# Optimization experiments

Measured on AMD Instinct MI355X. Metric: run time of the kernel, lower is better.

The kernel has to match this reference:

```python
import jax, jax.numpy as jnp
import numpy as np

N = 10000       # nodes
E = 160000      # edges
D_IN = 256      # in_channels (node feature dim)
H1, C = 8, 32   # conv1: 8 heads x 32 -> 256; conv2: 1 head x 32
MSG = 128       # msg_dim
TD = 128        # time encoder out_channels
ED = MSG + TD   # edge_dim = 256
HC1 = H1 * C    # 256


def _lin(key, shape, scale=0.05):
    return jax.random.normal(key, shape, dtype=jnp.float32) * scale


def setup_inputs() -> dict:
    key = jax.random.key(0)
    ks = jax.random.split(key, 32)
    inp = {}
    inp["x"] = jax.random.normal(ks[0], (N, D_IN), dtype=jnp.float32)
    inp["last_update"] = jax.random.uniform(ks[1], (N,), jnp.float32, 0.0, 1000.0)
    inp["edge_index"] = jax.random.randint(ks[2], (2, E), 0, N)
    inp["t"] = jax.random.uniform(ks[3], (E,), jnp.float32, 0.0, 1000.0)
    inp["msg"] = jax.random.normal(ks[4], (E, MSG), dtype=jnp.float32)
    # TimeEncoder: Linear(1, TD) then cos
    inp["time_w"] = _lin(ks[5], (TD, 1), 0.1)
    inp["time_b"] = jnp.zeros((TD,), jnp.float32)
    # conv1 (TransformerConv in=256, heads=8, per-head 32, edge_dim=256, concat=True)
    inp["Wq1"] = _lin(ks[6], (D_IN, HC1)); inp["bq1"] = jnp.zeros((HC1,), jnp.float32)
    inp["Wk1"] = _lin(ks[7], (D_IN, HC1)); inp["bk1"] = jnp.zeros((HC1,), jnp.float32)
    inp["Wv1"] = _lin(ks[8], (D_IN, HC1)); inp["bv1"] = jnp.zeros((HC1,), jnp.float32)
    inp["We1"] = _lin(ks[9], (ED, HC1))   # lin_edge has no bias in PyG
    inp["Ws1"] = _lin(ks[10], (D_IN, HC1)); inp["bs1"] = jnp.zeros((HC1,), jnp.float32)
    # conv2 (in=256, heads=1, per-head 32, concat=False)
    inp["Wq2"] = _lin(ks[11], (HC1, C)); inp["bq2"] = jnp.zeros((C,), jnp.float32)
    inp["Wk2"] = _lin(ks[12], (HC1, C)); inp["bk2"] = jnp.zeros((C,), jnp.float32)
    inp["Wv2"] = _lin(ks[13], (HC1, C)); inp["bv2"] = jnp.zeros((C,), jnp.float32)
    inp["We2"] = _lin(ks[14], (ED, C))
    inp["Ws2"] = _lin(ks[15], (HC1, C)); inp["bs2"] = jnp.zeros((C,), jnp.float32)
    return inp


def transformer_conv(x, src, dst, edge_attr, Wq, bq, Wk, bk, Wv, bv, We, Ws, bs, heads, ch, concat):
    n = x.shape[0]
    q = (x @ Wq + bq).reshape(n, heads, ch)
    k = (x @ Wk + bk).reshape(n, heads, ch)
    v = (x @ Wv + bv).reshape(n, heads, ch)
    e = (edge_attr @ We).reshape(-1, heads, ch)       # [E,H,C]
    ke = k[src] + e                                    # key_j + edge
    ve = v[src] + e                                    # value_j + edge
    alpha = jnp.einsum('ehc,ehc->eh', q[dst], ke) / jnp.sqrt(jnp.float32(ch))
    # segment softmax over incoming edges of each destination node
    amax = jax.ops.segment_max(alpha, dst, num_segments=n)   # -inf for empty segs
    ex = jnp.exp(alpha - amax[dst])
    den = jax.ops.segment_sum(ex, dst, num_segments=n)
    attn = ex / (den[dst] + 1e-16)                     # [E,H]
    out = jax.ops.segment_sum(attn[:, :, None] * ve, dst, num_segments=n)  # [N,H,C]
    out = out.reshape(n, heads * ch) if concat else out.mean(axis=1)
    return out + (x @ Ws + bs)                         # root skip connection


def reference(x, last_update, edge_index, t, msg, time_w, time_b,
              Wq1, bq1, Wk1, bk1, Wv1, bv1, We1, Ws1, bs1,
              Wq2, bq2, Wk2, bk2, Wv2, bv2, We2, Ws2, bs2):
    src, dst = edge_index[0], edge_index[1]
    rel_t = last_update[src] - t                       # [E]
    rel_t_enc = jnp.cos(rel_t[:, None] * time_w[:, 0][None, :] + time_b)  # [E,TD]
    edge_attr = jnp.concatenate([rel_t_enc, msg], axis=-1)                # [E,ED]
    h = jax.nn.relu(transformer_conv(x, src, dst, edge_attr,
                                     Wq1, bq1, Wk1, bk1, Wv1, bv1, We1, Ws1, bs1,
                                     H1, C, True))
    out = jax.nn.relu(transformer_conv(h, src, dst, edge_attr,
                                       Wq2, bq2, Wk2, bk2, Wv2, bv2, We2, Ws2, bs2,
                                       1, C, False))
    return out
```

## Files before the change

### kernel.cpp

```cpp
#include <hip/hip_runtime.h>
#include <math.h>

#define N_NODES 10000
#define N_EDGES 160000
#define RT1 157
#define RTE 2500
#define CONVX_T (RT1 * 64 * 32)
#define MAXSEG 16
#define SEGSTRIDE 576

static inline int ceildiv(int a, int b) { return (a + b - 1) / b; }

typedef float f32x4 __attribute__((ext_vector_type(4)));
typedef short bf16x8 __attribute__((ext_vector_type(8)));

__device__ __forceinline__ unsigned short f2bf(float f) {
  unsigned int u = __builtin_bit_cast(unsigned int, f);
  u += 0x7FFFu + ((u >> 16) & 1u);
  return (unsigned short)(u >> 16);
}
__device__ __forceinline__ float bf2f(unsigned short h) {
  unsigned int u = ((unsigned int)h) << 16;
  return __builtin_bit_cast(float, u);
}

__global__ void count_kernel(const int* __restrict__ dstp, int* __restrict__ deg, int E) {
  for (int i = blockIdx.x * blockDim.x + threadIdx.x; i < E; i += gridDim.x * blockDim.x)
    atomicAdd(&deg[dstp[i]], 1);
}

__global__ void scan_kernel(const int* __restrict__ deg, int* __restrict__ rowptr, int n) {
  __shared__ int part[1024];
  const int tid = threadIdx.x;
  const int CHK = 10;
  int base = tid * CHK;
  int loc[CHK];
  int s = 0;
#pragma unroll
  for (int j = 0; j < CHK; ++j) {
    int idx = base + j;
    int v = (idx < n) ? deg[idx] : 0;
    loc[j] = s; s += v;
  }
  part[tid] = s;
  __syncthreads();
  for (int off = 1; off < 1024; off <<= 1) {
    int y = (tid >= off) ? part[tid - off] : 0;
    __syncthreads();
    part[tid] += y;
    __syncthreads();
  }
  int pre = tid ? part[tid - 1] : 0;
#pragma unroll
  for (int j = 0; j < CHK; ++j) {
    int idx = base + j;
    if (idx < n) rowptr[idx] = pre + loc[j];
  }
  if (tid == 1023) rowptr[n] = part[1023];
}

__global__ void scatter_kernel(const float* __restrict__ lu, const float* __restrict__ tt,
                               const int* __restrict__ srcp, const int* __restrict__ dstp,
                               const int* __restrict__ rowptr, int* __restrict__ fill,
                               int* __restrict__ srcs, int* __restrict__ dsts,
                               int* __restrict__ eidA, float* __restrict__ rel_s, int E) {
  for (int e = blockIdx.x * blockDim.x + threadIdx.x; e < E; e += gridDim.x * blockDim.x) {
    int d = dstp[e], s = srcp[e];
    int pos = atomicAdd(&fill[d], 1);
    int slot = rowptr[d] + pos;
    srcs[slot] = s;
    dsts[slot] = d;
    eidA[slot] = e;
    rel_s[slot] = lu[s] - tt[e];
  }
}

__device__ __forceinline__ void wstore(const float* __restrict__ W, unsigned short* __restrict__ out,
                                       int Nin, int n_off, int NFtot, int k, int c) {
  int gc = n_off + c;
  int ks=k>>5, kg=(k>>3)&3, j=k&7, nf=gc>>4, ic=gc&15;
  out[(size_t)(ks*NFtot+nf)*512 + (ic+16*kg)*8 + j] = f2bf(W[(size_t)k*Nin + c]);
}

__global__ void conv_all_kernel(const float* __restrict__ x, unsigned short* __restrict__ xa,
                                const float* Wq1, const float* Wk1, const float* Wv1, const float* Ws1,
                                const float* We1, const float* Wq2, const float* Wk2, const float* Wv2,
                                const float* Ws2, const float* We2,
                                const float* bq1, const float* bk1, const float* bv1, const float* bs1,
                                const float* bq2, const float* bk2, const float* bv2, const float* bs2,
                                unsigned short* W1f, unsigned short* We1f, unsigned short* W2f,
                                unsigned short* We2f, float* bcat1, float* bcat2) {
  int t0 = blockIdx.x * blockDim.x + threadIdx.x;
  if (t0 < CONVX_T) {
    int i = t0 >> 5, k8 = t0 & 31;
    union { uint4 q; unsigned short s[8]; } u;
    if (i < N_NODES) {
      const float4* px = (const float4*)(x + (size_t)i * 256 + k8 * 8);
      float4 f0 = px[0], f1 = px[1];
      u.s[0]=f2bf(f0.x); u.s[1]=f2bf(f0.y); u.s[2]=f2bf(f0.z); u.s[3]=f2bf(f0.w);
      u.s[4]=f2bf(f1.x); u.s[5]=f2bf(f1.y); u.s[6]=f2bf(f1.z); u.s[7]=f2bf(f1.w);
    } else {
      u.q = make_uint4(0,0,0,0);
    }
    int rt=i>>6, rf=(i>>4)&3, ir=i&15, ks=k8>>2, kg=k8&3;
    *(uint4*)&xa[(size_t)rt*16384 + ks*2048 + rf*512 + (ir+16*kg)*8] = u.q;
    return;
  }
  int t = t0 - CONVX_T;
  if (t < 262144) {
    int w = t >> 16, r = t & 65535, k = r >> 8, c = r & 255;
    const float* W = (w == 0) ? Wq1 : (w == 1) ? Wk1 : (w == 2) ? Wv1 : Ws1;
    wstore(W, W1f, 256, w * 256, 64, k, c);
  } else if (t < 327680) {
    int r = t - 262144, k = r >> 8, c = r & 255;
    wstore(We1, We1f, 256, 0, 16, k, c);
  } else if (t < 360448) {
    int r = t - 327680, w = r >> 13, r2 = r & 8191, k = r2 >> 5, c = r2 & 31;
    const float* W = (w == 0) ? Wq2 : (w == 1) ? Wk2 : (w == 2) ? Wv2 : Ws2;
    wstore(W, W2f, 32, w * 32, 8, k, c);
  } else if (t < 368640) {
    int r = t - 360448, k = r >> 5, c = r & 31;
    wstore(We2, We2f, 32, 0, 4, k, c);
  } else if (t < 369792) {
    int r = t - 368640;
    if (r < 1024) {
      const float* b = (r < 256) ? bq1 : (r < 512) ? bk1 : (r < 768) ? bv1 : bs1;
      bcat1[r] = b[r & 255];
    } else {
      int r2 = r - 1024;
      const float* b = (r2 < 32) ? bq2 : (r2 < 64) ? bk2 : (r2 < 96) ? bv2 : bs2;
      bcat2[r2] = b[r2 & 31];
    }
  }
}

__global__ __launch_bounds__(512, 4)
void node1_gemm(const unsigned short* __restrict__ xa, const unsigned short* __restrict__ W1f,
                const float* __restrict__ bcat1, float* __restrict__ qf,
                unsigned short* __restrict__ kvb, float* __restrict__ sf) {
  __shared__ char ldsraw[32768];
  uint4* lds4 = (uint4*)ldsraw;
  const int tid = threadIdx.x;
  const int wid = tid >> 6, lane = tid & 63;
  const int fr0 = (lane >> 4) * 4;
  const int fc0 = lane & 15;
  const int rt0 = blockIdx.x % RT1;
  const int y = blockIdx.x / RT1;
  const int phase = rt0 & 7;

#pragma unroll
  for (int s = 0; s < 4; ++s)
    lds4[tid + s * 512] = *(const uint4*)(xa + (size_t)rt0 * 16384 + (size_t)(tid + s * 512) * 8);
  __syncthreads();

  f32x4 acc[4][2];
#pragma unroll
  for (int i = 0; i < 4; ++i)
#pragma unroll
    for (int j = 0; j < 2; ++j) acc[i][j] = (f32x4){0.f, 0.f, 0.f, 0.f};

  bf16x8 aN0, aN1, aN2, aN3, bN0, bN1;
  {
    const int ks = phase;
    aN0 = *(const bf16x8*)&lds4[ks * 256 + 0 * 64 + lane];
    aN1 = *(const bf16x8*)&lds4[ks * 256 + 1 * 64 + lane];
    aN2 = *(const bf16x8*)&lds4[ks * 256 + 2 * 64 + lane];
    aN3 = *(const bf16x8*)&lds4[ks * 256 + 3 * 64 + lane];
    bN0 = *(const bf16x8*)(W1f + ((size_t)(ks * 64 + y * 16 + wid * 2 + 0)) * 512 + (size_t)lane * 8);
    bN1 = *(const bf16x8*)(W1f + ((size_t)(ks * 64 + y * 16 + wid * 2 + 1)) * 512 + (size_t)lane * 8);
  }
#pragma unroll
  for (int ksi = 0; ksi < 8; ++ksi) {
    bf16x8 aC0 = aN0, aC1 = aN1, aC2 = aN2, aC3 = aN3;
    bf16x8 bC0 = bN0, bC1 = bN1;
    if (ksi < 7) {
      const int ks2 = (ksi + 1) ^ phase;
      aN0 = *(const bf16x8*)&lds4[ks2 * 256 + 0 * 64 + lane];
      aN1 = *(const bf16x8*)&lds4[ks2 * 256 + 1 * 64 + lane];
      aN2 = *(const bf16x8*)&lds4[ks2 * 256 + 2 * 64 + lane];
      aN3 = *(const bf16x8*)&lds4[ks2 * 256 + 3 * 64 + lane];
      bN0 = *(const bf16x8*)(W1f + ((size_t)(ks2 * 64 + y * 16 + wid * 2 + 0)) * 512 + (size_t)lane * 8);
      bN1 = *(const bf16x8*)(W1f + ((size_t)(ks2 * 64 + y * 16 + wid * 2 + 1)) * 512 + (size_t)lane * 8);
    }
    acc[0][0] = __builtin_amdgcn_mfma_f32_16x16x32_bf16(aC0, bC0, acc[0][0], 0, 0, 0);
    acc[1][0] = __builtin_amdgcn_mfma_f32_16x16x32_bf16(aC1, bC0, acc[1][0], 0, 0, 0);
    acc[2][0] = __builtin_amdgcn_mfma_f32_16x16x32_bf16(aC2, bC0, acc[2][0], 0, 0, 0);
    acc[3][0] = __builtin_amdgcn_mfma_f32_16x16x32_bf16(aC3, bC0, acc[3][0], 0, 0, 0);
    acc[0][1] = __builtin_amdgcn_mfma_f32_16x16x32_bf16(aC0, bC1, acc[0][1], 0, 0, 0);
    acc[1][1] = __builtin_amdgcn_mfma_f32_16x16x32_bf16(aC1, bC1, acc[1][1], 0, 0, 0);
    acc[2][1] = __builtin_amdgcn_mfma_f32_16x16x32_bf16(aC2, bC1, acc[2][1], 0, 0, 0);
    acc[3][1] = __builtin_amdgcn_mfma_f32_16x16x32_bf16(aC3, bC1, acc[3][1], 0, 0, 0);
  }

  bool bf16path;
  void* dstp_; int cstr_, dc0_, bcol0_;
  if (y == 0)      { bf16path = false; dstp_ = qf;  cstr_ = 256; dc0_ = 0;   bcol0_ = 0; }
  else if (y == 1) { bf16path = true;  dstp_ = kvb; cstr_ = 512; dc0_ = 0;   bcol0_ = 256; }
  else if (y == 2) { bf16path = true;  dstp_ = kvb; cstr_ = 512; dc0_ = 256; bcol0_ = 512; }
  else             { bf16path = false; dstp_ = sf;  cstr_ = 256; dc0_ = 0;   bcol0_ = 768; }
  if (!bf16path) {
    float* dst = (float*)dstp_;
    const int row0 = rt0 * 64 + fr0;
#pragma unroll
    for (int cf = 0; cf < 2; ++cf) {
      int c = wid * 32 + cf * 16 + fc0;
      float bv = bcat1[bcol0_ + c];
#pragma unroll
      for (int rf = 0; rf < 4; ++rf) {
#pragma unroll
        for (int j = 0; j < 4; ++j) {
          int r = row0 + rf * 16 + j;
          if (r < N_NODES) dst[(size_t)r * cstr_ + c] = acc[rf][cf][j] + bv;
        }
      }
    }
  } else {
    __syncthreads();
    unsigned short* cl = (unsigned short*)ldsraw;
    unsigned short* dst = (unsigned short*)dstp_;
    for (int pass = 0; pass < 4; ++pass) {
      if ((wid >> 1) == pass) {
#pragma unroll
        for (int cf = 0; cf < 2; ++cf) {
          int c = (wid & 1) * 32 + cf * 16 + fc0;
          float bv = bcat1[bcol0_ + pass * 64 + c];
#pragma unroll
          for (int rf = 0; rf < 4; ++rf)
#pragma unroll
            for (int j = 0; j < 4; ++j)
              cl[(fr0 + rf * 16 + j) * 72 + c] = f2bf(acc[rf][cf][j] + bv);
        }
      }
      __syncthreads();
      {
        int row = tid >> 3, cc = (tid & 7) * 8;
        int gr = rt0 * 64 + row;
        if (gr < N_NODES)
          *(uint4*)&dst[(size_t)gr * cstr_ + dc0_ + pass * 64 + cc] = *(const uint4*)&cl[row * 72 + cc];
      }
      __syncthreads();
    }
  }
}

__global__ __launch_bounds__(512, 4)
void edge_fused(const float* __restrict__ qf, const unsigned short* __restrict__ kvb,
                const unsigned short* __restrict__ We1f, const unsigned short* __restrict__ We2f,
                char* __restrict__ segrec, unsigned short* __restrict__ e2b,
                const float* __restrict__ rel_s, const float* __restrict__ tw,
                const float* __restrict__ tb, const float* __restrict__ msg,
                const int* __restrict__ eidA, const int* __restrict__ srcsA,
                const int* __restrict__ dstsA, const int* __restrict__ rowptr) {
  __shared__ char ldsraw[38912];
  uint4* lds4 = (uint4*)ldsraw;
  unsigned short* e1t = (unsigned short*)ldsraw;
  int* dseg     = (int*)(ldsraw + 33280);
  int* sseg     = (int*)(ldsraw + 33536);
  unsigned short* cl2 = (unsigned short*)(ldsraw + 33792);

  const int tid = threadIdx.x;
  const int wid = tid >> 6, lane = tid & 63;
  const int bx = blockIdx.x;
  const int fr0 = (lane >> 4) * 4;
  const int fc0 = lane & 15;
  const int rt0 = bx;

  const int rem = tid & 255;
  const int ksh = tid >> 8;
  float4 mA0, mA1, mB0, mB1;
  {
    const int arf = rem >> 6, ar2 = rem & 63, air = ar2 & 15, akg = ar2 >> 4;
    const int slot = rt0 * 64 + arf * 16 + air;
    int eorg = eidA[slot];
    const float4* pmA = (const float4*)(msg + (size_t)eorg * 128 + (size_t)(ksh * 4 + akg) * 8);
    mA0 = pmA[0]; mA1 = pmA[1];
    const float4* pmB = (const float4*)(msg + (size_t)eorg * 128 + (size_t)((2 + ksh) * 4 + akg) * 8);
    mB0 = pmB[0]; mB1 = pmB[1];
    if (tid < 64) {
      dseg[tid] = dstsA[rt0 * 64 + tid];
      sseg[tid] = srcsA[rt0 * 64 + tid];
    }
    float rl = rel_s[slot];
#pragma unroll
    for (int s = 0; s < 2; ++s) {
      int ks = ksh + s * 2;
      int k8 = ks * 4 + akg;
      const float4* twp = (const float4*)(tw + k8 * 8);
      const float4* tbp = (const float4*)(tb + k8 * 8);
      float4 w0 = twp[0], w1 = twp[1], b0 = tbp[0], b1 = tbp[1];
      union { uint4 q; unsigned short us[8]; } u;
      u.us[0]=f2bf(__cosf(rl*w0.x+b0.x)); u.us[1]=f2bf(__cosf(rl*w0.y+b0.y));
      u.us[2]=f2bf(__cosf(rl*w0.z+b0.z)); u.us[3]=f2bf(__cosf(rl*w0.w+b0.w));
      u.us[4]=f2bf(__cosf(rl*w1.x+b1.x)); u.us[5]=f2bf(__cosf(rl*w1.y+b1.y));
      u.us[6]=f2bf(__cosf(rl*w1.z+b1.z)); u.us[7]=f2bf(__cosf(rl*w1.w+b1.w));
      lds4[ks * 256 + rem] = u.q;
    }
  }
  __syncthreads();

  f32x4 acc[4][2];
  f32x4 acc2[4];
#pragma unroll
  for (int i = 0; i < 4; ++i) {
    acc2[i] = (f32x4){0.f, 0.f, 0.f, 0.f};
#pragma unroll
    for (int j = 0; j < 2; ++j) acc[i][j] = (f32x4){0.f, 0.f, 0.f, 0.f};
  }

  bf16x8 bN0, bN1, b2N;
  bN0 = *(const bf16x8*)(We1f + ((size_t)(0 * 16 + wid * 2 + 0)) * 512 + (size_t)lane * 8);
  bN1 = *(const bf16x8*)(We1f + ((size_t)(0 * 16 + wid * 2 + 1)) * 512 + (size_t)lane * 8);
  b2N = 0;
  if (wid < 2) b2N = *(const bf16x8*)(We2f + ((size_t)(0 * 4 + wid)) * 512 + (size_t)lane * 8);
#pragma unroll
  for (int ks = 0; ks < 4; ++ks) {
    bf16x8 bC0 = bN0, bC1 = bN1, b2C = b2N;
    if (ks < 3) {
      bN0 = *(const bf16x8*)(We1f + ((size_t)((ks + 1) * 16 + wid * 2 + 0)) * 512 + (size_t)lane * 8);
      bN1 = *(const bf16x8*)(We1f + ((size_t)((ks + 1) * 16 + wid * 2 + 1)) * 512 + (size_t)lane * 8);
      if (wid < 2) b2N = *(const bf16x8*)(We2f + ((size_t)((ks + 1) * 4 + wid)) * 512 + (size_t)lane * 8);
    }
    bf16x8 a0 = *(const bf16x8*)&lds4[ks * 256 + 0 * 64 + lane];
    bf16x8 a1 = *(const bf16x8*)&lds4[ks * 256 + 1 * 64 + lane];
    bf16x8 a2 = *(const bf16x8*)&lds4[ks * 256 + 2 * 64 + lane];
    bf16x8 a3 = *(const bf16x8*)&lds4[ks * 256 + 3 * 64 + lane];
    acc[0][0] = __builtin_amdgcn_mfma_f32_16x16x32_bf16(a0, bC0, acc[0][0], 0, 0, 0);
    acc[1][0] = __builtin_amdgcn_mfma_f32_16x16x32_bf16(a1, bC0, acc[1][0], 0, 0, 0);
    acc[2][0] = __builtin_amdgcn_mfma_f32_16x16x32_bf16(a2, bC0, acc[2][0], 0, 0, 0);
    acc[3][0] = __builtin_amdgcn_mfma_f32_16x16x32_bf16(a3, bC0, acc[3][0], 0, 0, 0);
    acc[0][1] = __builtin_amdgcn_mfma_f32_16x16x32_bf16(a0, bC1, acc[0][1], 0, 0, 0);
    acc[1][1] = __builtin_amdgcn_mfma_f32_16x16x32_bf16(a1, bC1, acc[1][1], 0, 0, 0);
    acc[2][1] = __builtin_amdgcn_mfma_f32_16x16x32_bf16(a2, bC1, acc[2][1], 0, 0, 0);
    acc[3][1] = __builtin_amdgcn_mfma_f32_16x16x32_bf16(a3, bC1, acc[3][1], 0, 0, 0);
    if (wid < 2) {
      acc2[0] = __builtin_amdgcn_mfma_f32_16x16x32_bf16(a0, b2C, acc2[0], 0, 0, 0);
      acc2[1] = __builtin_amdgcn_mfma_f32_16x16x32_bf16(a1, b2C, acc2[1], 0, 0, 0);
      acc2[2] = __builtin_amdgcn_mfma_f32_16x16x32_bf16(a2, b2C, acc2[2], 0, 0, 0);
      acc2[3] = __builtin_amdgcn_mfma_f32_16x16x32_bf16(a3, b2C, acc2[3], 0, 0, 0);
    }
  }

  bN0 = *(const bf16x8*)(We1f + ((size_t)(4 * 16 + wid * 2 + 0)) * 512 + (size_t)lane * 8);
  bN1 = *(const bf16x8*)(We1f + ((size_t)(4 * 16 + wid * 2 + 1)) * 512 + (size_t)lane * 8);
  if (wid < 2) b2N = *(const bf16x8*)(We2f + ((size_t)(4 * 4 + wid)) * 512 + (size_t)lane * 8);
  {
    union { uint4 q; unsigned short us[8]; } u;
    u.us[0]=f2bf(mA0.x); u.us[1]=f2bf(mA0.y); u.us[2]=f2bf(mA0.z); u.us[3]=f2bf(mA0.w);
    u.us[4]=f2bf(mA1.x); u.us[5]=f2bf(mA1.y); u.us[6]=f2bf(mA1.z); u.us[7]=f2bf(mA1.w);
    lds4[(4 + ksh) * 256 + rem] = u.q;
    u.us[0]=f2bf(mB0.x); u.us[1]=f2bf(mB0.y); u.us[2]=f2bf(mB0.z); u.us[3]=f2bf(mB0.w);
    u.us[4]=f2bf(mB1.x); u.us[5]=f2bf(mB1.y); u.us[6]=f2bf(mB1.z); u.us[7]=f2bf(mB1.w);
    lds4[(6 + ksh) * 256 + rem] = u.q;
  }
  __syncthreads();

#pragma unroll
  for (int ks = 4; ks < 8; ++ks) {
    bf16x8 bC0 = bN0, bC1 = bN1, b2C = b2N;
    if (ks < 7) {
      bN0 = *(const bf16x8*)(We1f + ((size_t)((ks + 1) * 16 + wid * 2 + 0)) * 512 + (size_t)lane * 8);
      bN1 = *(const bf16x8*)(We1f + ((size_t)((ks + 1) * 16 + wid * 2 + 1)) * 512 + (size_t)lane * 8);
      if (wid < 2) b2N = *(const bf16x8*)(We2f + ((size_t)((ks + 1) * 4 + wid)) * 512 + (size_t)lane * 8);
    }
    bf16x8 a0 = *(const bf16x8*)&lds4[ks * 256 + 0 * 64 + lane];
    bf16x8 a1 = *(const bf16x8*)&lds4[ks * 256 + 1 * 64 + lane];
    bf16x8 a2 = *(const bf16x8*)&lds4[ks * 256 + 2 * 64 + lane];
    bf16x8 a3 = *(const bf16x8*)&lds4[ks * 256 + 3 * 64 + lane];
    acc[0][0] = __builtin_amdgcn_mfma_f32_16x16x32_bf16(a0, bC0, acc[0][0], 0, 0, 0);
    acc[1][0] = __builtin_amdgcn_mfma_f32_16x16x32_bf16(a1, bC0, acc[1][0], 0, 0, 0);
    acc[2][0] = __builtin_amdgcn_mfma_f32_16x16x32_bf16(a2, bC0, acc[2][0], 0, 0, 0);
    acc[3][0] = __builtin_amdgcn_mfma_f32_16x16x32_bf16(a3, bC0, acc[3][0], 0, 0, 0);
    acc[0][1] = __builtin_amdgcn_mfma_f32_16x16x32_bf16(a0, bC1, acc[0][1], 0, 0, 0);
    acc[1][1] = __builtin_amdgcn_mfma_f32_16x16x32_bf16(a1, bC1, acc[1][1], 0, 0, 0);
    acc[2][1] = __builtin_amdgcn_mfma_f32_16x16x32_bf16(a2, bC1, acc[2][1], 0, 0, 0);
    acc[3][1] = __builtin_amdgcn_mfma_f32_16x16x32_bf16(a3, bC1, acc[3][1], 0, 0, 0);
    if (wid < 2) {
      acc2[0] = __builtin_amdgcn_mfma_f32_16x16x32_bf16(a0, b2C, acc2[0], 0, 0, 0);
      acc2[1] = __builtin_amdgcn_mfma_f32_16x16x32_bf16(a1, b2C, acc2[1], 0, 0, 0);
      acc2[2] = __builtin_amdgcn_mfma_f32_16x16x32_bf16(a2, b2C, acc2[2], 0, 0, 0);
      acc2[3] = __builtin_amdgcn_mfma_f32_16x16x32_bf16(a3, b2C, acc2[3], 0, 0, 0);
    }
  }

  __syncthreads();
#pragma unroll
  for (int cf = 0; cf < 2; ++cf)
#pragma unroll
    for (int rf = 0; rf < 4; ++rf)
#pragma unroll
      for (int j = 0; j < 4; ++j)
        e1t[(fr0 + rf * 16 + j) * 260 + wid * 32 + cf * 16 + fc0] = f2bf(acc[rf][cf][j]);
  if (wid < 2) {
#pragma unroll
    for (int rf = 0; rf < 4; ++rf)
#pragma unroll
      for (int j = 0; j < 4; ++j)
        cl2[(fr0 + rf * 16 + j) * 40 + wid * 16 + fc0] = f2bf(acc2[rf][j]);
  }
  __syncthreads();

  if (tid < 256) {
    int row = tid >> 2, cc = (tid & 3) * 8;
    *(uint4*)&e2b[(size_t)(rt0 * 64 + row) * 32 + cc] = *(const uint4*)&cl2[row * 40 + cc];
  }

  {
    const int base = wid * 8;
    const int rgj = bx * 8 + wid;
    int d8[8], s8[8];
#pragma unroll
    for (int t = 0; t < 8; ++t) { d8[t] = dseg[base + t]; s8[t] = sseg[base + t]; }

    float4 q8[8]; ushort4 k8[8], e8[8];
#pragma unroll
    for (int t = 0; t < 8; ++t) {
      q8[t] = *(const float4*)&qf[(size_t)d8[t] * 256 + lane * 4];
      k8[t] = *(const ushort4*)&kvb[(size_t)s8[t] * 512 + lane * 4];
      e8[t] = *(const ushort4*)&e1t[(base + t) * 260 + lane * 4];
    }
    float sc[8];
#pragma unroll
    for (int t = 0; t < 8; ++t) {
      float p = q8[t].x * (bf2f(k8[t].x) + bf2f(e8[t].x))
              + q8[t].y * (bf2f(k8[t].y) + bf2f(e8[t].y))
              + q8[t].z * (bf2f(k8[t].z) + bf2f(e8[t].z))
              + q8[t].w * (bf2f(k8[t].w) + bf2f(e8[t].w));
      p += __shfl_xor(p, 1); p += __shfl_xor(p, 2); p += __shfl_xor(p, 4);
      sc[t] = p * 0.17677669529663687f;
    }
    ushort4 v8[8];
#pragma unroll
    for (int t = 0; t < 8; ++t)
      v8[t] = *(const ushort4*)&kvb[(size_t)s8[t] * 512 + 256 + lane * 4];

    float m8[8], w8[8];
#pragma unroll
    for (int t = 0; t < 8; ++t) {
      float mm = sc[t];
#pragma unroll
      for (int u = 0; u < 8; ++u)
        if (d8[u] == d8[t]) mm = fmaxf(mm, sc[u]);
      m8[t] = mm;
      w8[t] = __expf(sc[t] - mm);
    }
#pragma unroll
    for (int t = 0; t < 8; ++t) {
      bool first = (t == 0) || (d8[t - 1] != d8[t]);
      if (first && (lane & 7) == 0) {
        float den = 0.f;
#pragma unroll
        for (int u = 0; u < 8; ++u)
          if (d8[u] == d8[t]) den += w8[u];
        int j = rgj - (rowptr[d8[t]] >> 3);
        if (j < MAXSEG) {
          float* rec = (float*)(segrec + ((size_t)d8[t] * MAXSEG + j) * SEGSTRIDE);
          rec[128 + (lane >> 3)] = m8[t];
          rec[136 + (lane >> 3)] = den;
        }
      }
    }
    f32x4 pacc = (f32x4){0.f, 0.f, 0.f, 0.f};
    int cur = d8[0];
#pragma unroll
    for (int t = 0; t < 8; ++t) {
      if (d8[t] != cur) {
        int j = rgj - (rowptr[cur] >> 3);
        if (j < MAXSEG) {
          unsigned short* pp = (unsigned short*)(segrec + ((size_t)cur * MAXSEG + j) * SEGSTRIDE);
          ushort4 o;
          o.x = f2bf(pacc[0]); o.y = f2bf(pacc[1]); o.z = f2bf(pacc[2]); o.w = f2bf(pacc[3]);
          *(ushort4*)&pp[lane * 4] = o;
        }
        pacc = (f32x4){0.f, 0.f, 0.f, 0.f};
        cur = d8[t];
      }
      pacc[0] += w8[t] * (bf2f(v8[t].x) + bf2f(e8[t].x));
      pacc[1] += w8[t] * (bf2f(v8[t].y) + bf2f(e8[t].y));
      pacc[2] += w8[t] * (bf2f(v8[t].z) + bf2f(e8[t].z));
      pacc[3] += w8[t] * (bf2f(v8[t].w) + bf2f(e8[t].w));
    }
    {
      int j = rgj - (rowptr[cur] >> 3);
      if (j < MAXSEG) {
        unsigned short* pp = (unsigned short*)(segrec + ((size_t)cur * MAXSEG + j) * SEGSTRIDE);
        ushort4 o;
        o.x = f2bf(pacc[0]); o.y = f2bf(pacc[1]); o.z = f2bf(pacc[2]); o.w = f2bf(pacc[3]);
        *(ushort4*)&pp[lane * 4] = o;
      }
    }
  }
}

__global__ __launch_bounds__(256)
void node2_fused(const char* __restrict__ segrec, const int* __restrict__ rowptr,
                 const float* __restrict__ sf, const unsigned short* __restrict__ W2f,
                 const float* __restrict__ bcat2, float* __restrict__ qkvs2) {
  __shared__ unsigned short haL[8 * 2048];
  const int tid = threadIdx.x;
  const int wid = tid >> 6, lane = tid & 63;
  const int rt0 = blockIdx.x;

  {
    const int nl = tid >> 2;
    const int n = rt0 * 64 + nl;
    const int cb = (tid & 3) * 64;
    const int rf = (nl >> 4) & 3, ir = nl & 15;
    if (n < N_NODES) {
      const int beg = rowptr[n], end = rowptr[n + 1];
      int s0 = 0, span = 0;
      if (beg < end) {
        s0 = beg >> 3;
        span = ((end - 1) >> 3) - s0 + 1;
        if (span > MAXSEG) span = MAXSEG;
      }
#pragma unroll
      for (int cc = 0; cc < 4; ++cc) {
        const int c0 = cb + cc * 16;
        const int h = c0 >> 5;
        float o[16];
        if (span == 0) {
#pragma unroll
          for (int q = 0; q < 16; ++q) o[q] = 0.f;
        } else {
          float M = -INFINITY;
          for (int j = 0; j < span; ++j) {
            const float* rec = (const float*)(segrec + ((size_t)n * MAXSEG + j) * SEGSTRIDE);
            M = fmaxf(M, rec[128 + h]);
          }
          float den = 0.f;
#pragma unroll
          for (int q = 0; q < 16; ++q) o[q] = 0.f;
          for (int j = 0; j < span; ++j) {
            const float* rec = (const float*)(segrec + ((size_t)n * MAXSEG + j) * SEGSTRIDE);
            float scj = __expf(rec[128 + h] - M);
            den += scj * rec[136 + h];
            const unsigned short* pp = (const unsigned short*)rec;
#pragma unroll
            for (int q4 = 0; q4 < 4; ++q4) {
              ushort4 p4 = *(const ushort4*)&pp[c0 + q4 * 4];
              o[q4*4+0] += scj * bf2f(p4.x); o[q4*4+1] += scj * bf2f(p4.y);
              o[q4*4+2] += scj * bf2f(p4.z); o[q4*4+3] += scj * bf2f(p4.w);
            }
          }
          const float inv = 1.f / (den + 1e-16f);
#pragma unroll
          for (int q = 0; q < 16; ++q) o[q] *= inv;
        }
#pragma unroll
        for (int q4 = 0; q4 < 4; ++q4) {
          const int c = c0 + q4 * 4;
          float4 sk = *(const float4*)&sf[(size_t)n * 256 + c];
          ushort4 w4;
          w4.x = f2bf(fmaxf(o[q4*4+0] + sk.x, 0.f));
          w4.y = f2bf(fmaxf(o[q4*4+1] + sk.y, 0.f));
          w4.z = f2bf(fmaxf(o[q4*4+2] + sk.z, 0.f));
          w4.w = f2bf(fmaxf(o[q4*4+3] + sk.w, 0.f));
          int ks = c >> 5, kg = (c >> 3) & 3, j = c & 7;
          *(ushort4*)&haL[ks * 2048 + rf * 512 + (ir + 16 * kg) * 8 + j] = w4;
        }
      }
    } else {
#pragma unroll
      for (int cc = 0; cc < 4; ++cc) {
        const int c0 = cb + cc * 16;
#pragma unroll
        for (int q4 = 0; q4 < 4; ++q4) {
          const int c = c0 + q4 * 4;
          int ks = c >> 5, kg = (c >> 3) & 3, j = c & 7;
          ushort4 z; z.x = z.y = z.z = z.w = 0;
          *(ushort4*)&haL[ks * 2048 + rf * 512 + (ir + 16 * kg) * 8 + j] = z;
        }
      }
    }
  }
  __syncthreads();

  f32x4 acc[4][2];
#pragma unroll
  for (int i = 0; i < 4; ++i)
#pragma unroll
    for (int j = 0; j < 2; ++j) acc[i][j] = (f32x4){0.f, 0.f, 0.f, 0.f};

#pragma unroll
  for (int ks = 0; ks < 8; ++ks) {
    bf16x8 a[4], b[2];
#pragma unroll
    for (int rf = 0; rf < 4; ++rf)
      a[rf] = *(const bf16x8*)&haL[ks * 2048 + (rf * 64 + lane) * 8];
#pragma unroll
    for (int cf = 0; cf < 2; ++cf)
      b[cf] = *(const bf16x8*)(W2f + ((size_t)(ks * 8 + wid * 2 + cf)) * 512 + (size_t)lane * 8);
#pragma unroll
    for (int rf = 0; rf < 4; ++rf)
#pragma unroll
      for (int cf = 0; cf < 2; ++cf)
        acc[rf][cf] = __builtin_amdgcn_mfma_f32_16x16x32_bf16(a[rf], b[cf], acc[rf][cf], 0, 0, 0);
  }

  const int row0 = rt0 * 64 + ((lane >> 4) * 4);
  const int cb2 = wid * 32 + (lane & 15);
#pragma unroll
  for (int cf = 0; cf < 2; ++cf) {
    int c = cb2 + cf * 16;
    float bv = bcat2[c];
#pragma unroll
    for (int rf = 0; rf < 4; ++rf) {
#pragma unroll
      for (int j = 0; j < 4; ++j) {
        int r = row0 + rf * 16 + j;
        if (r < N_NODES) qkvs2[(size_t)r * 128 + c] = acc[rf][cf][j] + bv;
      }
    }
  }
}

__global__ __launch_bounds__(256)
void attn2_kernel(const float* __restrict__ qkvs2, const unsigned short* __restrict__ e2b,
                  const int* __restrict__ srcs, const int* __restrict__ rowptr,
                  float* __restrict__ outp) {
  const int n = blockIdx.x * 4 + (threadIdx.x >> 6);
  if (n >= N_NODES) return;
  const int lane = threadIdx.x & 63;
  const int c = lane & 31;
  const int beg = rowptr[n], end = rowptr[n + 1];
  const float qv = qkvs2[(size_t)n * 128 + c];

  float m0=-INFINITY,d0=0,x0=0;
  float m1=-INFINITY,d1=0,x1=0;
  float m2=-INFINITY,d2=0,x2=0;
  float m3=-INFINITY,d3=0,x3=0;

  auto step = [&](int i, float& m, float& d, float& a) {
    const int s = srcs[i];
    const float ev = bf2f(e2b[(size_t)i * 32 + c]);
    float p = qv * (qkvs2[(size_t)s * 128 + 32 + c] + ev);
    const float v = qkvs2[(size_t)s * 128 + 64 + c] + ev;
#pragma unroll
    for (int off = 16; off; off >>= 1) p += __shfl_xor(p, off);
    p *= 0.17677669529663687f;
    const float mn = fmaxf(m, p);
    const float sc = __expf(m - mn), w = __expf(p - mn);
    d = d * sc + w; a = a * sc + w * v; m = mn;
  };

  int i = beg;
  for (; i + 3 < end; i += 4) {
    step(i, m0, d0, x0);
    step(i + 1, m1, d1, x1);
    step(i + 2, m2, d2, x2);
    step(i + 3, m3, d3, x3);
  }
  for (; i < end; ++i) step(i, m0, d0, x0);

  auto merge = [&](float& m, float& d, float& a, float mB, float dB, float b) {
    if (mB == -INFINITY) return;
    const float M = fmaxf(m, mB);
    const float sA = __expf(m - M), sB = __expf(mB - M);
    d = d * sA + dB * sB; a = a * sA + b * sB; m = M;
  };
  merge(m0, d0, x0, m1, d1, x1);
  merge(m2, d2, x2, m3, d3, x3);
  merge(m0, d0, x0, m2, d2, x2);

  if (lane < 32) {
    float o = x0 / (d0 + 1e-16f) + qkvs2[(size_t)n * 128 + 96 + c];
    outp[(size_t)n * 32 + c] = fmaxf(o, 0.f);
  }
}

extern "C" void kernel_launch(void* const* d_in, const int* in_sizes, int n_in,
                              void* d_out, int out_size, void* d_ws, size_t ws_size,
                              hipStream_t stream) {
  const float* x   = (const float*)d_in[0];
  const float* lu  = (const float*)d_in[1];
  const int*   ei  = (const int*)d_in[2];
  const float* tt  = (const float*)d_in[3];
  const float* msg = (const float*)d_in[4];
  const float* tw  = (const float*)d_in[5];
  const float* tb  = (const float*)d_in[6];
  const float* Wq1 = (const float*)d_in[7];  const float* bq1 = (const float*)d_in[8];
  const float* Wk1 = (const float*)d_in[9];  const float* bk1 = (const float*)d_in[10];
  const float* Wv1 = (const float*)d_in[11]; const float* bv1 = (const float*)d_in[12];
  const float* We1 = (const float*)d_in[13];
  const float* Ws1 = (const float*)d_in[14]; const float* bs1 = (const float*)d_in[15];
  const float* Wq2 = (const float*)d_in[16]; const float* bq2 = (const float*)d_in[17];
  const float* Wk2 = (const float*)d_in[18]; const float* bk2 = (const float*)d_in[19];
  const float* Wv2 = (const float*)d_in[20]; const float* bv2 = (const float*)d_in[21];
  const float* We2 = (const float*)d_in[22];
  const float* Ws2 = (const float*)d_in[23]; const float* bs2 = (const float*)d_in[24];

  const int* srcp = ei;
  const int* dstp = ei + N_EDGES;

  char* p = (char*)d_ws;
  auto alloc = [&](size_t bytes) -> char* {
    char* r = p;
    p += (bytes + 255) & ~(size_t)255;
    return r;
  };
  int*   deg     = (int*)alloc((size_t)N_NODES * 4);
  int*   fill    = (int*)alloc((size_t)N_NODES * 4);
  int*   rowptr  = (int*)alloc((size_t)(N_NODES + 1) * 4);
  int*   srcs    = (int*)alloc((size_t)N_EDGES * 4);
  int*   dsts    = (int*)alloc((size_t)N_EDGES * 4);
  int*   eidA    = (int*)alloc((size_t)N_EDGES * 4);
  float* rel_s   = (float*)alloc((size_t)N_EDGES * 4);
  unsigned short* xa   = (unsigned short*)alloc((size_t)RT1 * 32768);
  unsigned short* W1f  = (unsigned short*)alloc((size_t)8 * 64 * 1024);
  unsigned short* We1f = (unsigned short*)alloc((size_t)8 * 16 * 1024);
  unsigned short* W2f  = (unsigned short*)alloc((size_t)8 * 8 * 1024);
  unsigned short* We2f = (unsigned short*)alloc((size_t)8 * 4 * 1024);
  float* bcat1  = (float*)alloc(1024 * 4);
  float* bcat2  = (float*)alloc(128 * 4);
  float* qf     = (float*)alloc((size_t)N_NODES * 256 * 4);
  unsigned short* kvb = (unsigned short*)alloc((size_t)N_NODES * 512 * 2);
  float* sf     = (float*)alloc((size_t)N_NODES * 256 * 4);
  char*  segrec = (char*)alloc((size_t)N_NODES * MAXSEG * SEGSTRIDE);
  float* qkvs2  = (float*)alloc((size_t)N_NODES * 128 * 4);
  unsigned short* e2b = (unsigned short*)alloc((size_t)N_EDGES * 32 * 2);
  float* outp   = (float*)d_out;

  hipMemsetAsync(deg, 0, (size_t)N_NODES * 4, stream);
  hipMemsetAsync(fill, 0, (size_t)N_NODES * 4, stream);

  count_kernel<<<625, 256, 0, stream>>>(dstp, deg, N_EDGES);
  scan_kernel<<<1, 1024, 0, stream>>>(deg, rowptr, N_NODES);
  scatter_kernel<<<625, 256, 0, stream>>>(lu, tt, srcp, dstp, rowptr, fill,
                                          srcs, dsts, eidA, rel_s, N_EDGES);

  conv_all_kernel<<<ceildiv(CONVX_T + 369792, 256), 256, 0, stream>>>(
      x, xa, Wq1, Wk1, Wv1, Ws1, We1, Wq2, Wk2, Wv2, Ws2, We2,
      bq1, bk1, bv1, bs1, bq2, bk2, bv2, bs2,
      W1f, We1f, W2f, We2f, bcat1, bcat2);

  node1_gemm<<<RT1 * 4, 512, 0, stream>>>(xa, W1f, bcat1, qf, kvb, sf);

  edge_fused<<<RTE, 512, 0, stream>>>(
      qf, kvb, We1f, We2f, segrec, e2b,
      rel_s, tw, tb, msg, eidA, srcs, dsts, rowptr);

  node2_fused<<<RT1, 256, 0, stream>>>(segrec, rowptr, sf, W2f, bcat2, qkvs2);
  attn2_kernel<<<ceildiv(N_NODES, 4), 256, 0, stream>>>(qkvs2, e2b, srcs, rowptr, outp);
}
```

Before: 172.2 us.

## Stage all edge A-tiles upfront, stagger K order, dedupe q loads, halve attn2 waves

In edge_fused, the msg tiles are converted and written to LDS together with the time-encoding tiles before a single barrier. This removes the mid-loop barrier and the two-phase K loop. The K loop now runs in a per-block rotated order (ks XOR blockIdx&7) with register prefetch of both LDS A fragments and global weight fragments, aiming to spread weight reads and overlap loads with MFMA. Query rows are reused when consecutive edges share a destination, and attn2 maps one node per 32 lanes instead of 64, so no half-wave sits idle. The cost is more live registers and all global msg loads moving before the barrier.

```diff
diff --git a/kernel.cpp b/kernel.cpp
--- a/kernel.cpp
+++ b/kernel.cpp
@@ -264,23 +264,19 @@
   const int fr0 = (lane >> 4) * 4;
   const int fc0 = lane & 15;
   const int rt0 = bx;
-
-  const int rem = tid & 255;
-  const int ksh = tid >> 8;
-  float4 mA0, mA1, mB0, mB1;
+  const int phase = bx & 7;
+
   {
+    const int rem = tid & 255;
+    const int ksh = tid >> 8;
     const int arf = rem >> 6, ar2 = rem & 63, air = ar2 & 15, akg = ar2 >> 4;
     const int slot = rt0 * 64 + arf * 16 + air;
+    float rl = rel_s[slot];
     int eorg = eidA[slot];
-    const float4* pmA = (const float4*)(msg + (size_t)eorg * 128 + (size_t)(ksh * 4 + akg) * 8);
-    mA0 = pmA[0]; mA1 = pmA[1];
-    const float4* pmB = (const float4*)(msg + (size_t)eorg * 128 + (size_t)((2 + ksh) * 4 + akg) * 8);
-    mB0 = pmB[0]; mB1 = pmB[1];
     if (tid < 64) {
       dseg[tid] = dstsA[rt0 * 64 + tid];
       sseg[tid] = srcsA[rt0 * 64 + tid];
     }
-    float rl = rel_s[slot];
 #pragma unroll
     for (int s = 0; s < 2; ++s) {
       int ks = ksh + s * 2;
@@ -295,6 +291,17 @@
       u.us[6]=f2bf(__cosf(rl*w1.z+b1.z)); u.us[7]=f2bf(__cosf(rl*w1.w+b1.w));
       lds4[ks * 256 + rem] = u.q;
     }
+#pragma unroll
+    for (int s = 0; s < 2; ++s) {
+      int ks = 4 + ksh + s * 2;
+      int k8 = ks * 4 + akg;
+      const float4* pm = (const float4*)(msg + (size_t)eorg * 128 + (size_t)(k8 - 16) * 8);
+      float4 f0 = pm[0], f1 = pm[1];
+      union { uint4 q; unsigned short us[8]; } u;
+      u.us[0]=f2bf(f0.x); u.us[1]=f2bf(f0.y); u.us[2]=f2bf(f0.z); u.us[3]=f2bf(f0.w);
+      u.us[4]=f2bf(f1.x); u.us[5]=f2bf(f1.y); u.us[6]=f2bf(f1.z); u.us[7]=f2bf(f1.w);
+      lds4[ks * 256 + rem] = u.q;
+    }
   }
   __syncthreads();
 
@@ -307,78 +314,45 @@
     for (int j = 0; j < 2; ++j) acc[i][j] = (f32x4){0.f, 0.f, 0.f, 0.f};
   }
 
-  bf16x8 bN0, bN1, b2N;
-  bN0 = *(const bf16x8*)(We1f + ((size_t)(0 * 16 + wid * 2 + 0)) * 512 + (size_t)lane * 8);
-  bN1 = *(const bf16x8*)(We1f + ((size_t)(0 * 16 + wid * 2 + 1)) * 512 + (size_t)lane * 8);
-  b2N = 0;
-  if (wid < 2) b2N = *(const bf16x8*)(We2f + ((size_t)(0 * 4 + wid)) * 512 + (size_t)lane * 8);
-#pragma unroll
-  for (int ks = 0; ks < 4; ++ks) {
+  bf16x8 aN0, aN1, aN2, aN3, bN0, bN1, b2N;
+  {
+    const int ks = phase;
+    aN0 = *(const bf16x8*)&lds4[ks * 256 + 0 * 64 + lane];
+    aN1 = *(const bf16x8*)&lds4[ks * 256 + 1 * 64 + lane];
+    aN2 = *(const bf16x8*)&lds4[ks * 256 + 2 * 64 + lane];
+    aN3 = *(const bf16x8*)&lds4[ks * 256 + 3 * 64 + lane];
+    bN0 = *(const bf16x8*)(We1f + ((size_t)(ks * 16 + wid * 2 + 0)) * 512 + (size_t)lane * 8);
+    bN1 = *(const bf16x8*)(We1f + ((size_t)(ks * 16 + wid * 2 + 1)) * 512 + (size_t)lane * 8);
+    b2N = 0;
+    if (wid < 2) b2N = *(const bf16x8*)(We2f + ((size_t)(ks * 4 + wid)) * 512 + (size_t)lane * 8);
+  }
+#pragma unroll
+  for (int ksi = 0; ksi < 8; ++ksi) {
+    bf16x8 aC0 = aN0, aC1 = aN1, aC2 = aN2, aC3 = aN3;
     bf16x8 bC0 = bN0, bC1 = bN1, b2C = b2N;
-    if (ks < 3) {
-      bN0 = *(const bf16x8*)(We1f + ((size_t)((ks + 1) * 16 + wid * 2 + 0)) * 512 + (size_t)lane * 8);
-      bN1 = *(const bf16x8*)(We1f + ((size_t)((ks + 1) * 16 + wid * 2 + 1)) * 512 + (size_t)lane * 8);
-      if (wid < 2) b2N = *(const bf16x8*)(We2f + ((size_t)((ks + 1) * 4 + wid)) * 512 + (size_t)lane * 8);
-    }
-    bf16x8 a0 = *(const bf16x8*)&lds4[ks * 256 + 0 * 64 + lane];
-    bf16x8 a1 = *(const bf16x8*)&lds4[ks * 256 + 1 * 64 + lane];
-    bf16x8 a2 = *(const bf16x8*)&lds4[ks * 256 + 2 * 64 + lane];
-    bf16x8 a3 = *(const bf16x8*)&lds4[ks * 256 + 3 * 64 + lane];
-    acc[0][0] = __builtin_amdgcn_mfma_f32_16x16x32_bf16(a0, bC0, acc[0][0], 0, 0, 0);
-    acc[1][0] = __builtin_amdgcn_mfma_f32_16x16x32_bf16(a1, bC0, acc[1][0], 0, 0, 0);
-    acc[2][0] = __builtin_amdgcn_mfma_f32_16x16x32_bf16(a2, bC0, acc[2][0], 0, 0, 0);
-    acc[3][0] = __builtin_amdgcn_mfma_f32_16x16x32_bf16(a3, bC0, acc[3][0], 0, 0, 0);
-    acc[0][1] = __builtin_amdgcn_mfma_f32_16x16x32_bf16(a0, bC1, acc[0][1], 0, 0, 0);
-    acc[1][1] = __builtin_amdgcn_mfma_f32_16x16x32_bf16(a1, bC1, acc[1][1], 0, 0, 0);
-    acc[2][1] = __builtin_amdgcn_mfma_f32_16x16x32_bf16(a2, bC1, acc[2][1], 0, 0, 0);
-    acc[3][1] = __builtin_amdgcn_mfma_f32_16x16x32_bf16(a3, bC1, acc[3][1], 0, 0, 0);
+    if (ksi < 7) {
+      const int ks2 = (ksi + 1) ^ phase;
+      aN0 = *(const bf16x8*)&lds4[ks2 * 256 + 0 * 64 + lane];
+      aN1 = *(const bf16x8*)&lds4[ks2 * 256 + 1 * 64 + lane];
+      aN2 = *(const bf16x8*)&lds4[ks2 * 256 + 2 * 64 + lane];
+      aN3 = *(const bf16x8*)&lds4[ks2 * 256 + 3 * 64 + lane];
+      bN0 = *(const bf16x8*)(We1f + ((size_t)(ks2 * 16 + wid * 2 + 0)) * 512 + (size_t)lane * 8);
+      bN1 = *(const bf16x8*)(We1f + ((size_t)(ks2 * 16 + wid * 2 + 1)) * 512 + (size_t)lane * 8);
+      if (wid < 2) b2N = *(const bf16x8*)(We2f + ((size_t)(ks2 * 4 + wid)) * 512 + (size_t)lane * 8);
+    }
+    acc[0][0] = __builtin_amdgcn_mfma_f32_16x16x32_bf16(aC0, bC0, acc[0][0], 0, 0, 0);
+    acc[1][0] = __builtin_amdgcn_mfma_f32_16x16x32_bf16(aC1, bC0, acc[1][0], 0, 0, 0);
+    acc[2][0] = __builtin_amdgcn_mfma_f32_16x16x32_bf16(aC2, bC0, acc[2][0], 0, 0, 0);
+    acc[3][0] = __builtin_amdgcn_mfma_f32_16x16x32_bf16(aC3, bC0, acc[3][0], 0, 0, 0);
+    acc[0][1] = __builtin_amdgcn_mfma_f32_16x16x32_bf16(aC0, bC1, acc[0][1], 0, 0, 0);
+    acc[1][1] = __builtin_amdgcn_mfma_f32_16x16x32_bf16(aC1, bC1, acc[1][1], 0, 0, 0);
+    acc[2][1] = __builtin_amdgcn_mfma_f32_16x16x32_bf16(aC2, bC1, acc[2][1], 0, 0, 0);
+    acc[3][1] = __builtin_amdgcn_mfma_f32_16x16x32_bf16(aC3, bC1, acc[3][1], 0, 0, 0);
     if (wid < 2) {
-      acc2[0] = __builtin_amdgcn_mfma_f32_16x16x32_bf16(a0, b2C, acc2[0], 0, 0, 0);
-      acc2[1] = __builtin_amdgcn_mfma_f32_16x16x32_bf16(a1, b2C, acc2[1], 0, 0, 0);
-      acc2[2] = __builtin_amdgcn_mfma_f32_16x16x32_bf16(a2, b2C, acc2[2], 0, 0, 0);
-      acc2[3] = __builtin_amdgcn_mfma_f32_16x16x32_bf16(a3, b2C, acc2[3], 0, 0, 0);
-    }
-  }
-
-  bN0 = *(const bf16x8*)(We1f + ((size_t)(4 * 16 + wid * 2 + 0)) * 512 + (size_t)lane * 8);
-  bN1 = *(const bf16x8*)(We1f + ((size_t)(4 * 16 + wid * 2 + 1)) * 512 + (size_t)lane * 8);
-  if (wid < 2) b2N = *(const bf16x8*)(We2f + ((size_t)(4 * 4 + wid)) * 512 + (size_t)lane * 8);
-  {
-    union { uint4 q; unsigned short us[8]; } u;
-    u.us[0]=f2bf(mA0.x); u.us[1]=f2bf(mA0.y); u.us[2]=f2bf(mA0.z); u.us[3]=f2bf(mA0.w);
-    u.us[4]=f2bf(mA1.x); u.us[5]=f2bf(mA1.y); u.us[6]=f2bf(mA1.z); u.us[7]=f2bf(mA1.w);
-    lds4[(4 + ksh) * 256 + rem] = u.q;
-    u.us[0]=f2bf(mB0.x); u.us[1]=f2bf(mB0.y); u.us[2]=f2bf(mB0.z); u.us[3]=f2bf(mB0.w);
-    u.us[4]=f2bf(mB1.x); u.us[5]=f2bf(mB1.y); u.us[6]=f2bf(mB1.z); u.us[7]=f2bf(mB1.w);
-    lds4[(6 + ksh) * 256 + rem] = u.q;
-  }
-  __syncthreads();
-
-#pragma unroll
-  for (int ks = 4; ks < 8; ++ks) {
-    bf16x8 bC0 = bN0, bC1 = bN1, b2C = b2N;
-    if (ks < 7) {
-      bN0 = *(const bf16x8*)(We1f + ((size_t)((ks + 1) * 16 + wid * 2 + 0)) * 512 + (size_t)lane * 8);
-      bN1 = *(const bf16x8*)(We1f + ((size_t)((ks + 1) * 16 + wid * 2 + 1)) * 512 + (size_t)lane * 8);
-      if (wid < 2) b2N = *(const bf16x8*)(We2f + ((size_t)((ks + 1) * 4 + wid)) * 512 + (size_t)lane * 8);
-    }
-    bf16x8 a0 = *(const bf16x8*)&lds4[ks * 256 + 0 * 64 + lane];
-    bf16x8 a1 = *(const bf16x8*)&lds4[ks * 256 + 1 * 64 + lane];
-    bf16x8 a2 = *(const bf16x8*)&lds4[ks * 256 + 2 * 64 + lane];
-    bf16x8 a3 = *(const bf16x8*)&lds4[ks * 256 + 3 * 64 + lane];
-    acc[0][0] = __builtin_amdgcn_mfma_f32_16x16x32_bf16(a0, bC0, acc[0][0], 0, 0, 0);
-    acc[1][0] = __builtin_amdgcn_mfma_f32_16x16x32_bf16(a1, bC0, acc[1][0], 0, 0, 0);
-    acc[2][0] = __builtin_amdgcn_mfma_f32_16x16x32_bf16(a2, bC0, acc[2][0], 0, 0, 0);
-    acc[3][0] = __builtin_amdgcn_mfma_f32_16x16x32_bf16(a3, bC0, acc[3][0], 0, 0, 0);
-    acc[0][1] = __builtin_amdgcn_mfma_f32_16x16x32_bf16(a0, bC1, acc[0][1], 0, 0, 0);
-    acc[1][1] = __builtin_amdgcn_mfma_f32_16x16x32_bf16(a1, bC1, acc[1][1], 0, 0, 0);
-    acc[2][1] = __builtin_amdgcn_mfma_f32_16x16x32_bf16(a2, bC1, acc[2][1], 0, 0, 0);
-    acc[3][1] = __builtin_amdgcn_mfma_f32_16x16x32_bf16(a3, bC1, acc[3][1], 0, 0, 0);
-    if (wid < 2) {
-      acc2[0] = __builtin_amdgcn_mfma_f32_16x16x32_bf16(a0, b2C, acc2[0], 0, 0, 0);
-      acc2[1] = __builtin_amdgcn_mfma_f32_16x16x32_bf16(a1, b2C, acc2[1], 0, 0, 0);
-      acc2[2] = __builtin_amdgcn_mfma_f32_16x16x32_bf16(a2, b2C, acc2[2], 0, 0, 0);
-      acc2[3] = __builtin_amdgcn_mfma_f32_16x16x32_bf16(a3, b2C, acc2[3], 0, 0, 0);
+      acc2[0] = __builtin_amdgcn_mfma_f32_16x16x32_bf16(aC0, b2C, acc2[0], 0, 0, 0);
+      acc2[1] = __builtin_amdgcn_mfma_f32_16x16x32_bf16(aC1, b2C, acc2[1], 0, 0, 0);
+      acc2[2] = __builtin_amdgcn_mfma_f32_16x16x32_bf16(aC2, b2C, acc2[2], 0, 0, 0);
+      acc2[3] = __builtin_amdgcn_mfma_f32_16x16x32_bf16(aC3, b2C, acc2[3], 0, 0, 0);
     }
   }
 
@@ -411,12 +385,18 @@
 #pragma unroll
     for (int t = 0; t < 8; ++t) { d8[t] = dseg[base + t]; s8[t] = sseg[base + t]; }
 
-    float4 q8[8]; ushort4 k8[8], e8[8];
+    ushort4 k8[8], e8[8];
 #pragma unroll
     for (int t = 0; t < 8; ++t) {
-      q8[t] = *(const float4*)&qf[(size_t)d8[t] * 256 + lane * 4];
       k8[t] = *(const ushort4*)&kvb[(size_t)s8[t] * 512 + lane * 4];
       e8[t] = *(const ushort4*)&e1t[(base + t) * 260 + lane * 4];
+    }
+    float4 q8[8];
+    q8[0] = *(const float4*)&qf[(size_t)d8[0] * 256 + lane * 4];
+#pragma unroll
+    for (int t = 1; t < 8; ++t) {
+      if (d8[t] == d8[t - 1]) q8[t] = q8[t - 1];
+      else q8[t] = *(const float4*)&qf[(size_t)d8[t] * 256 + lane * 4];
     }
     float sc[8];
 #pragma unroll
@@ -507,10 +487,9 @@
     const int rf = (nl >> 4) & 3, ir = nl & 15;
     if (n < N_NODES) {
       const int beg = rowptr[n], end = rowptr[n + 1];
-      int s0 = 0, span = 0;
+      int span = 0;
       if (beg < end) {
-        s0 = beg >> 3;
-        span = ((end - 1) >> 3) - s0 + 1;
+        span = ((end - 1) >> 3) - (beg >> 3) + 1;
         if (span > MAXSEG) span = MAXSEG;
       }
 #pragma unroll
@@ -618,10 +597,9 @@
 void attn2_kernel(const float* __restrict__ qkvs2, const unsigned short* __restrict__ e2b,
                   const int* __restrict__ srcs, const int* __restrict__ rowptr,
                   float* __restrict__ outp) {
-  const int n = blockIdx.x * 4 + (threadIdx.x >> 6);
+  const int n = blockIdx.x * 8 + (threadIdx.x >> 5);
   if (n >= N_NODES) return;
-  const int lane = threadIdx.x & 63;
-  const int c = lane & 31;
+  const int c = threadIdx.x & 31;
   const int beg = rowptr[n], end = rowptr[n + 1];
   const float qv = qkvs2[(size_t)n * 128 + c];
 
@@ -662,10 +640,8 @@
   merge(m2, d2, x2, m3, d3, x3);
   merge(m0, d0, x0, m2, d2, x2);
 
-  if (lane < 32) {
-    float o = x0 / (d0 + 1e-16f) + qkvs2[(size_t)n * 128 + 96 + c];
-    outp[(size_t)n * 32 + c] = fmaxf(o, 0.f);
-  }
+  float o = x0 / (d0 + 1e-16f) + qkvs2[(size_t)n * 128 + 96 + c];
+  outp[(size_t)n * 32 + c] = fmaxf(o, 0.f);
 }
 
 extern "C" void kernel_launch(void* const* d_in, const int* in_sizes, int n_in,
@@ -740,5 +716,5 @@
       rel_s, tw, tb, msg, eidA, srcs, dsts, rowptr);
 
   node2_fused<<<RT1, 256, 0, stream>>>(segrec, rowptr, sf, W2f, bcat2, qkvs2);
-  attn2_kernel<<<ceildiv(N_NODES, 4), 256, 0, stream>>>(qkvs2, e2b, srcs, rowptr, outp);
-}
+  attn2_kernel<<<ceildiv(N_NODES, 8), 256, 0, stream>>>(qkvs2, e2b, srcs, rowptr, outp);
+}
```

Result: faster. 164.5 us (-4.5%).
